# Kernel optimization log

Hardware: AMD Instinct MI355X
Metric: run time of the kernel (lower is better)

Reference implementation:

```python
import jax, jax.numpy as jnp
import numpy as np
from jax import lax

B, N, D = 256, 257, 768   # batch, 1+num_patches, token dim
K = 8                     # top-k concepts per image
V = 10000                 # codebook size
KMEANS_ITERS = 4
BETA_EMA = 0.99


def _l2norm(x, eps=1e-12):
    return x / jnp.maximum(jnp.linalg.norm(x, axis=-1, keepdims=True), eps)


def setup_inputs() -> dict:
    key = jax.random.key(0)
    k1, k2, k3 = jax.random.split(key, 3)
    tokens = jax.random.normal(k1, (B, N, D), dtype=jnp.float32)
    visual_concepts = jax.random.normal(k2, (V, 2, D), dtype=jnp.float32)
    topk_indices = jax.random.randint(k3, (B, K), 0, V)
    return {"tokens": tokens, "visual_concepts": visual_concepts, "topk_indices": topk_indices}


def reference(tokens, visual_concepts, topk_indices):
    # gather per-image codebook entries: [b, k, 2, d]
    vc_g = _l2norm(visual_concepts[topk_indices])
    tp = tokens[:, 1:]  # drop CLS -> [b, n, d]

    def step(centroids, _):
        sim = jnp.einsum('bnd,bkcd->bnkc', tp, centroids)          # [b,n,k,2]
        assign = jnp.argmax(sim, axis=-1).astype(tp.dtype)          # [b,n,k] in {0,1}
        c1 = jnp.einsum('bnd,bnk->bkd', tp, assign)
        c0 = jnp.einsum('bnd,bnk->bkd', tp, 1.0 - assign)
        centroids = _l2norm(jnp.stack([c0, c1], axis=2))            # [b,k,2,d]
        return centroids, assign

    centroids, assigns = lax.scan(step, vc_g, None, length=KMEANS_ITERS)
    assignments = assigns[-1]  # torch returns the last iteration's assignments

    # NOTE: in the torch code `centroids` aliases the gathered `visual_concepts`
    # and is mutated in-place, so beta*visual_concepts + (1-beta)*centroids == centroids.
    concepts_ema = BETA_EMA * centroids + (1.0 - BETA_EMA) * centroids

    # torch scatter_reduce_ with index shape (b*k, 1, 1) only scatters src[:, 0, 0]
    # into visual_concepts[idx, 0, 0] with reduce='sum' (include_self=True).
    src = concepts_ema.reshape(-1, 2, D)
    idx = topk_indices.reshape(-1)
    vc_new = visual_concepts.at[idx, 0, 0].add(src[:, 0, 0])
    vc_new = _l2norm(vc_new)
    return assignments, vc_new
```

## Files before the change

### kernel.cpp

```cpp
#include <hip/hip_runtime.h>
#include <hip/hip_bf16.h>

#define BB 256
#define NN 257
#define NT 256
#define DD 768
#define KC 8
#define VV 10000
#define ITERS 4

#define CHD 32
#define NCH (DD / CHD)
#define CF4 (CHD / 4)
#define CSTR 193

__device__ __forceinline__ float waveReduceSum(float v) {
#pragma unroll
    for (int off = 32; off > 0; off >>= 1)
        v += __shfl_xor(v, off, 64);
    return v;
}

__device__ __forceinline__ float dot4chain(float4 a, float4 c, float acc) {
    return fmaf(a.w, c.w, fmaf(a.z, c.z, fmaf(a.y, c.y, fmaf(a.x, c.x, acc))));
}

__device__ __forceinline__ void gld16(const float* g, void* lds) {
    __builtin_amdgcn_global_load_lds(
        (const __attribute__((address_space(1))) void*)g,
        (__attribute__((address_space(3))) void*)lds,
        16, 0, 0);
}

__global__ __launch_bounds__(1024, 4) void kmeans_kernel(
    const float* __restrict__ tokens,
    const float* __restrict__ vc,
    const int* __restrict__ topk,
    float* __restrict__ out_assign,
    float* __restrict__ delta)
{
    __shared__ float4 cent4[16 * CSTR];
    __shared__ float4 tbuf4[3 * NT * CF4];
    __shared__ int sidx[KC];

    float* centf = (float*)cent4;
    float (*maskF)[KC] = (float (*)[KC])tbuf4;

    const int b = blockIdx.x;
    const int t = threadIdx.x;
    const int lane = t & 63;
    const int wave = t >> 6;

    if (t < KC) sidx[t] = topk[b * KC + t];
    __syncthreads();

    {
        const int r = wave;
        const int k = r >> 1, c = r & 1;
        const float* src = vc + ((size_t)sidx[k] * 2 + c) * DD;
        float vals[12];
        float ss = 0.f;
#pragma unroll
        for (int j = 0; j < 12; ++j) {
            vals[j] = src[lane + 64 * j];
            ss = fmaf(vals[j], vals[j], ss);
        }
        ss = waveReduceSum(ss);
        float iv = 1.0f / fmaxf(sqrtf(ss), 1e-12f);
#pragma unroll
        for (int j = 0; j < 12; ++j)
            centf[r * 772 + lane + 64 * j] = vals[j] * iv;
    }
    __syncthreads();

    const float* tpb = tokens + ((size_t)b * NN + 1) * DD;

    const int tok = t & 255;
    const int g   = t >> 8;
    const int s7  = tok & 7;

    const int slotA = wave * 128 + lane;
    const int slotB = slotA + 64;
    const float* gbaseA = tpb + (size_t)(slotA >> 3) * DD + 4 * ((slotA & 7) ^ ((slotA >> 3) & 7));
    const float* gbaseB = tpb + (size_t)(slotB >> 3) * DD + 4 * ((slotB & 7) ^ ((slotB >> 3) & 7));

    float tsum_reg = 0.f;

    for (int it = 0; it < ITERS; ++it) {
        float acc[4] = {0.f, 0.f, 0.f, 0.f};

        gld16(gbaseA,       (void*)(tbuf4 + wave * 128));
        gld16(gbaseB,       (void*)(tbuf4 + wave * 128 + 64));
        gld16(gbaseA + CHD, (void*)(tbuf4 + 2048 + wave * 128));
        gld16(gbaseB + CHD, (void*)(tbuf4 + 2048 + wave * 128 + 64));

#pragma unroll 1
        for (int cix = 0; cix < NCH - 1; ++cix) {
            asm volatile("s_waitcnt vmcnt(2)" ::: "memory");
            __builtin_amdgcn_s_barrier();
            __builtin_amdgcn_sched_barrier(0);
            if (cix + 2 < NCH) {
                const int nb = (cix + 2) % 3;
                gld16(gbaseA + (cix + 2) * CHD, (void*)(tbuf4 + nb * 2048 + wave * 128));
                gld16(gbaseB + (cix + 2) * CHD, (void*)(tbuf4 + nb * 2048 + wave * 128 + 64));
            }
            {
                const float4* tb = tbuf4 + (cix % 3) * 2048 + (tok << 3);
                const float4* cr = cent4 + (g * 4) * CSTR + (cix << 3);
#pragma unroll
                for (int j4 = 0; j4 < CF4; ++j4) {
                    float4 a  = tb[j4 ^ s7];
                    float4 c0 = cr[j4];
                    float4 c1 = cr[CSTR + j4];
                    float4 c2 = cr[2 * CSTR + j4];
                    float4 c3 = cr[3 * CSTR + j4];
                    acc[0] = dot4chain(a, c0, acc[0]);
                    acc[1] = dot4chain(a, c1, acc[1]);
                    acc[2] = dot4chain(a, c2, acc[2]);
                    acc[3] = dot4chain(a, c3, acc[3]);
                }
            }
        }
        __syncthreads();
        {
            const int cix = NCH - 1;
            const float4* tb = tbuf4 + (cix % 3) * 2048 + (tok << 3);
            const float4* cr = cent4 + (g * 4) * CSTR + (cix << 3);
#pragma unroll
            for (int j4 = 0; j4 < CF4; ++j4) {
                float4 a  = tb[j4 ^ s7];
                float4 c0 = cr[j4];
                float4 c1 = cr[CSTR + j4];
                float4 c2 = cr[2 * CSTR + j4];
                float4 c3 = cr[3 * CSTR + j4];
                acc[0] = dot4chain(a, c0, acc[0]);
                acc[1] = dot4chain(a, c1, acc[1]);
                acc[2] = dot4chain(a, c2, acc[2]);
                acc[3] = dot4chain(a, c3, acc[3]);
            }
        }

        {
            float2 mf;
            mf.x = (acc[1] > acc[0]) ? 1.f : 0.f;
            mf.y = (acc[3] > acc[2]) ? 1.f : 0.f;
            *(float2*)&maskF[tok][2 * g] = mf;
        }
        __syncthreads();

        if (it == ITERS - 1 && t < NT) {
            const float4* mf4 = (const float4*)&maskF[t][0];
            float4* op = (float4*)(out_assign + ((size_t)b * NT + t) * KC);
            op[0] = mf4[0]; op[1] = mf4[1];
        }

        if (t < DD) {
            const int d = t;
            const float* col = tpb + d;
            const float4* mrow = (const float4*)&maskF[0][0];
            float a0 = 0.f, a1 = 0.f, a2 = 0.f, a3 = 0.f;
            float a4 = 0.f, a5 = 0.f, a6 = 0.f, a7 = 0.f;
            float tr = 0.f;
            for (int n0 = 0; n0 < NT; n0 += 16) {
                float v[16];
#pragma unroll
                for (int u = 0; u < 16; ++u)
                    v[u] = col[(size_t)(n0 + u) * DD];
#pragma unroll
                for (int u = 0; u < 16; ++u) {
                    float4 ma = mrow[2 * (n0 + u)];
                    float4 mb = mrow[2 * (n0 + u) + 1];
                    a0 = fmaf(v[u], ma.x, a0);
                    a1 = fmaf(v[u], ma.y, a1);
                    a2 = fmaf(v[u], ma.z, a2);
                    a3 = fmaf(v[u], ma.w, a3);
                    a4 = fmaf(v[u], mb.x, a4);
                    a5 = fmaf(v[u], mb.y, a5);
                    a6 = fmaf(v[u], mb.z, a6);
                    a7 = fmaf(v[u], mb.w, a7);
                    if (it == 0) tr += v[u];
                }
            }
            if (it == 0) tsum_reg = tr;
            centf[ 1 * 772 + d] = a0;  centf[ 0 * 772 + d] = tsum_reg - a0;
            centf[ 3 * 772 + d] = a1;  centf[ 2 * 772 + d] = tsum_reg - a1;
            centf[ 5 * 772 + d] = a2;  centf[ 4 * 772 + d] = tsum_reg - a2;
            centf[ 7 * 772 + d] = a3;  centf[ 6 * 772 + d] = tsum_reg - a3;
            centf[ 9 * 772 + d] = a4;  centf[ 8 * 772 + d] = tsum_reg - a4;
            centf[11 * 772 + d] = a5;  centf[10 * 772 + d] = tsum_reg - a5;
            centf[13 * 772 + d] = a6;  centf[12 * 772 + d] = tsum_reg - a6;
            centf[15 * 772 + d] = a7;  centf[14 * 772 + d] = tsum_reg - a7;
        }
        __syncthreads();

        {
            const int r = wave;
            float vals[12];
            float ss = 0.f;
#pragma unroll
            for (int j = 0; j < 12; ++j) {
                vals[j] = centf[r * 772 + lane + 64 * j];
                ss = fmaf(vals[j], vals[j], ss);
            }
            ss = waveReduceSum(ss);
            float iv = 1.0f / fmaxf(sqrtf(ss), 1e-12f);
#pragma unroll
            for (int j = 0; j < 12; ++j)
                centf[r * 772 + lane + 64 * j] = vals[j] * iv;
        }
        __syncthreads();
    }

    if (t < KC) {
        atomicAdd(delta + sidx[t], centf[(2 * t) * 772]);
    }
}

__global__ __launch_bounds__(1024) void vcnorm_kernel(
    const float* __restrict__ vc,
    const float* __restrict__ delta,
    float* __restrict__ out)
{
    const int t = threadIdx.x;
    const int lane = t & 63;
    const int wave = t >> 6;
    const int r = blockIdx.x * 16 + wave;
    if (r >= 2 * VV) return;
    const int v = r >> 1;
    const int c = r & 1;
    const float* src = vc + (size_t)r * DD;
    float4 x[3];
#pragma unroll
    for (int j = 0; j < 3; ++j)
        x[j] = *(const float4*)(src + (lane + 64 * j) * 4);
    if (c == 0 && lane == 0) x[0].x += delta[v];
    float ss = 0.f;
#pragma unroll
    for (int j = 0; j < 3; ++j)
        ss += x[j].x * x[j].x + x[j].y * x[j].y + x[j].z * x[j].z + x[j].w * x[j].w;
    ss = waveReduceSum(ss);
    float iv = 1.0f / fmaxf(sqrtf(ss), 1e-12f);
    float* dst = out + (size_t)r * DD;
#pragma unroll
    for (int j = 0; j < 3; ++j) {
        float4 y = make_float4(x[j].x * iv, x[j].y * iv, x[j].z * iv, x[j].w * iv);
        *(float4*)(dst + (lane + 64 * j) * 4) = y;
    }
}

extern "C" void kernel_launch(void* const* d_in, const int* in_sizes, int n_in,
                              void* d_out, int out_size, void* d_ws, size_t ws_size,
                              hipStream_t stream) {
    const float* tokens = (const float*)d_in[0];
    const float* vc     = (const float*)d_in[1];
    const int*   topk   = (const int*)d_in[2];
    float* out          = (float*)d_out;
    float* assignments  = out;
    float* vcnew        = out + (size_t)BB * NT * KC;
    float* delta        = (float*)d_ws;

    hipMemsetAsync(delta, 0, VV * sizeof(float), stream);
    hipLaunchKernelGGL(kmeans_kernel, dim3(BB), dim3(1024), 0, stream,
                       tokens, vc, topk, assignments, delta);
    hipLaunchKernelGGL(vcnorm_kernel, dim3((2 * VV + 15) / 16), dim3(1024), 0, stream,
                       vc, delta, vcnew);
}
```

Measured before the change: 648.6 us.

## Stage centroid-update token reads through double-buffered LDS using producer waves

The centroid accumulation phase previously read token columns straight from global memory, one thread per feature dimension. It now streams the tokens in 16-token chunks into a double-buffered LDS area with async global_load_lds. The four waves beyond the 768 compute threads act as producers, and barriers synchronise each chunk. The goal is to hide global latency and get coalesced loads, at the cost of more LDS, more barriers, and four waves idle in the compute loop.

New measurement: 692.7 us. +6.8%, slower.

```diff
diff --git a/kernel.cpp b/kernel.cpp
--- a/kernel.cpp
+++ b/kernel.cpp
@@ -13,6 +13,10 @@
 #define NCH (DD / CHD)
 #define CF4 (CHD / 4)
 #define CSTR 193
+
+#define ATOK 16
+#define ANCH (NT / ATOK)
+#define ACHF (ATOK * DD)
 
 __device__ __forceinline__ float waveReduceSum(float v) {
 #pragma unroll
@@ -40,11 +44,12 @@
     float* __restrict__ delta)
 {
     __shared__ float4 cent4[16 * CSTR];
-    __shared__ float4 tbuf4[3 * NT * CF4];
+    __shared__ float4 tbuf4[6656];
     __shared__ int sidx[KC];
 
     float* centf = (float*)cent4;
-    float (*maskF)[KC] = (float (*)[KC])tbuf4;
+    float* tfl   = (float*)tbuf4;
+    float (*maskF)[KC] = (float (*)[KC])((char*)tbuf4 + 98304);
 
     const int b = blockIdx.x;
     const int t = threadIdx.x;
@@ -83,6 +88,10 @@
     const int slotB = slotA + 64;
     const float* gbaseA = tpb + (size_t)(slotA >> 3) * DD + 4 * ((slotA & 7) ^ ((slotA >> 3) & 7));
     const float* gbaseB = tpb + (size_t)(slotB >> 3) * DD + 4 * ((slotB & 7) ^ ((slotB >> 3) & 7));
+
+    const int p = wave - 12;
+    const float* asrc = tpb + (size_t)(p >= 0 ? p : 0) * 12 * 256 + lane * 4;
+    float* adst = tfl + (p >= 0 ? p : 0) * 12 * 256;
 
     float tsum_reg = 0.f;
 
@@ -154,33 +163,58 @@
             op[0] = mf4[0]; op[1] = mf4[1];
         }
 
+        if (wave >= 12) {
+#pragma unroll
+            for (int j = 0; j < 12; ++j)
+                gld16(asrc + j * 256, (void*)(adst + j * 256));
+#pragma unroll
+            for (int j = 0; j < 12; ++j)
+                gld16(asrc + ACHF + j * 256, (void*)(adst + ACHF + j * 256));
+        }
+
+        float a0 = 0.f, a1 = 0.f, a2 = 0.f, a3 = 0.f;
+        float a4 = 0.f, a5 = 0.f, a6 = 0.f, a7 = 0.f;
+        float tr = 0.f;
+
+#pragma unroll 1
+        for (int c = 0; c < ANCH; ++c) {
+            if (wave >= 12) {
+                if (c < ANCH - 1) asm volatile("s_waitcnt vmcnt(12)" ::: "memory");
+                else              asm volatile("s_waitcnt vmcnt(0)"  ::: "memory");
+            }
+            __builtin_amdgcn_s_barrier();
+            __builtin_amdgcn_sched_barrier(0);
+            if (t < DD) {
+                const float* cb = tfl + (c & 1) * ACHF + t;
+#pragma unroll
+                for (int i = 0; i < ATOK; ++i) {
+                    float v = cb[i * DD];
+                    const float4* mr = (const float4*)&maskF[c * ATOK + i][0];
+                    float4 ma = mr[0];
+                    float4 mb = mr[1];
+                    a0 = fmaf(v, ma.x, a0);
+                    a1 = fmaf(v, ma.y, a1);
+                    a2 = fmaf(v, ma.z, a2);
+                    a3 = fmaf(v, ma.w, a3);
+                    a4 = fmaf(v, mb.x, a4);
+                    a5 = fmaf(v, mb.y, a5);
+                    a6 = fmaf(v, mb.z, a6);
+                    a7 = fmaf(v, mb.w, a7);
+                    if (it == 0) tr += v;
+                }
+            }
+            __builtin_amdgcn_s_barrier();
+            __builtin_amdgcn_sched_barrier(0);
+            if (wave >= 12 && c + 2 < ANCH) {
+#pragma unroll
+                for (int j = 0; j < 12; ++j)
+                    gld16(asrc + (size_t)(c + 2) * ACHF + j * 256,
+                          (void*)(adst + (c & 1) * ACHF + j * 256));
+            }
+        }
+
         if (t < DD) {
             const int d = t;
-            const float* col = tpb + d;
-            const float4* mrow = (const float4*)&maskF[0][0];
-            float a0 = 0.f, a1 = 0.f, a2 = 0.f, a3 = 0.f;
-            float a4 = 0.f, a5 = 0.f, a6 = 0.f, a7 = 0.f;
-            float tr = 0.f;
-            for (int n0 = 0; n0 < NT; n0 += 16) {
-                float v[16];
-#pragma unroll
-                for (int u = 0; u < 16; ++u)
-                    v[u] = col[(size_t)(n0 + u) * DD];
-#pragma unroll
-                for (int u = 0; u < 16; ++u) {
-                    float4 ma = mrow[2 * (n0 + u)];
-                    float4 mb = mrow[2 * (n0 + u) + 1];
-                    a0 = fmaf(v[u], ma.x, a0);
-                    a1 = fmaf(v[u], ma.y, a1);
-                    a2 = fmaf(v[u], ma.z, a2);
-                    a3 = fmaf(v[u], ma.w, a3);
-                    a4 = fmaf(v[u], mb.x, a4);
-                    a5 = fmaf(v[u], mb.y, a5);
-                    a6 = fmaf(v[u], mb.z, a6);
-                    a7 = fmaf(v[u], mb.w, a7);
-                    if (it == 0) tr += v[u];
-                }
-            }
             if (it == 0) tsum_reg = tr;
             centf[ 1 * 772 + d] = a0;  centf[ 0 * 772 + d] = tsum_reg - a0;
             centf[ 3 * 772 + d] = a1;  centf[ 2 * 772 + d] = tsum_reg - a1;
```

## Remap token/group threads so each wave consumes only its own loads, drop barriers

Applied to the files above, without the earlier changes.

Changes the thread mapping so the four centroid-group threads for a token sit in the same wave (tok = t>>2, g = t&3). Each wave then reads only the token slots it fetched into LDS itself, so the per-chunk block-wide barrier is replaced by a wave-local vmcnt wait. The last-chunk special case is folded into the loop, and the mask buffer gets its own LDS array so it no longer aliases the token staging buffer. The cost is that lanes in a wave now read four different centroid rows instead of broadcasting one, which may add LDS bank pressure.

Measured after the change: 732.6 us. +12.9%, slower.

```diff
diff --git a/kernel.cpp b/kernel.cpp
--- a/kernel.cpp
+++ b/kernel.cpp
@@ -40,11 +40,12 @@
     float* __restrict__ delta)
 {
     __shared__ float4 cent4[16 * CSTR];
-    __shared__ float4 tbuf4[3 * NT * CF4];
+    __shared__ float4 tbuf4[3 * 2048];
+    __shared__ float4 maskF4[NT * 2];
     __shared__ int sidx[KC];
 
-    float* centf = (float*)cent4;
-    float (*maskF)[KC] = (float (*)[KC])tbuf4;
+    float* centf  = (float*)cent4;
+    float* maskFf = (float*)maskF4;
 
     const int b = blockIdx.x;
     const int t = threadIdx.x;
@@ -75,8 +76,8 @@
 
     const float* tpb = tokens + ((size_t)b * NN + 1) * DD;
 
-    const int tok = t & 255;
-    const int g   = t >> 8;
+    const int tok = t >> 2;
+    const int g   = t & 3;
     const int s7  = tok & 7;
 
     const int slotA = wave * 128 + lane;
@@ -95,9 +96,9 @@
         gld16(gbaseB + CHD, (void*)(tbuf4 + 2048 + wave * 128 + 64));
 
 #pragma unroll 1
-        for (int cix = 0; cix < NCH - 1; ++cix) {
-            asm volatile("s_waitcnt vmcnt(2)" ::: "memory");
-            __builtin_amdgcn_s_barrier();
+        for (int cix = 0; cix < NCH; ++cix) {
+            if (cix < NCH - 1) asm volatile("s_waitcnt vmcnt(2)" ::: "memory");
+            else               asm volatile("s_waitcnt vmcnt(0)" ::: "memory");
             __builtin_amdgcn_sched_barrier(0);
             if (cix + 2 < NCH) {
                 const int nb = (cix + 2) % 3;
@@ -121,43 +122,23 @@
                 }
             }
         }
-        __syncthreads();
-        {
-            const int cix = NCH - 1;
-            const float4* tb = tbuf4 + (cix % 3) * 2048 + (tok << 3);
-            const float4* cr = cent4 + (g * 4) * CSTR + (cix << 3);
-#pragma unroll
-            for (int j4 = 0; j4 < CF4; ++j4) {
-                float4 a  = tb[j4 ^ s7];
-                float4 c0 = cr[j4];
-                float4 c1 = cr[CSTR + j4];
-                float4 c2 = cr[2 * CSTR + j4];
-                float4 c3 = cr[3 * CSTR + j4];
-                acc[0] = dot4chain(a, c0, acc[0]);
-                acc[1] = dot4chain(a, c1, acc[1]);
-                acc[2] = dot4chain(a, c2, acc[2]);
-                acc[3] = dot4chain(a, c3, acc[3]);
-            }
-        }
 
         {
             float2 mf;
             mf.x = (acc[1] > acc[0]) ? 1.f : 0.f;
             mf.y = (acc[3] > acc[2]) ? 1.f : 0.f;
-            *(float2*)&maskF[tok][2 * g] = mf;
+            *(float2*)(maskFf + tok * KC + 2 * g) = mf;
         }
         __syncthreads();
 
         if (it == ITERS - 1 && t < NT) {
-            const float4* mf4 = (const float4*)&maskF[t][0];
             float4* op = (float4*)(out_assign + ((size_t)b * NT + t) * KC);
-            op[0] = mf4[0]; op[1] = mf4[1];
+            op[0] = maskF4[2 * t]; op[1] = maskF4[2 * t + 1];
         }
 
         if (t < DD) {
             const int d = t;
             const float* col = tpb + d;
-            const float4* mrow = (const float4*)&maskF[0][0];
             float a0 = 0.f, a1 = 0.f, a2 = 0.f, a3 = 0.f;
             float a4 = 0.f, a5 = 0.f, a6 = 0.f, a7 = 0.f;
             float tr = 0.f;
@@ -168,8 +149,8 @@
                     v[u] = col[(size_t)(n0 + u) * DD];
 #pragma unroll
                 for (int u = 0; u < 16; ++u) {
-                    float4 ma = mrow[2 * (n0 + u)];
-                    float4 mb = mrow[2 * (n0 + u) + 1];
+                    float4 ma = maskF4[2 * (n0 + u)];
+                    float4 mb = maskF4[2 * (n0 + u) + 1];
                     a0 = fmaf(v[u], ma.x, a0);
                     a1 = fmaf(v[u], ma.y, a1);
                     a2 = fmaf(v[u], ma.z, a2);
```
